# Kernel optimization log

Hardware: AMD Instinct MI355X
Metric: run time of the kernel (lower is better)

The kernel has to match this reference:

```python
import jax, jax.numpy as jnp
import numpy as np

N_HEADS = 16
MASK_NEG = -1e32


def setup_inputs() -> dict:
    key = jax.random.key(0)
    k0, k1, k2, k3, k4 = jax.random.split(key, 5)
    B, S, D = 8, 1024, 1024
    return {
        "q": jax.random.normal(k0, (B, S, D), dtype=jnp.float32),
        "k": jax.random.normal(k1, (B, S, D), dtype=jnp.float32),
        "v1": jax.random.normal(k2, (B, S, D), dtype=jnp.float32),
        "v2": jax.random.normal(k3, (B, S, D), dtype=jnp.float32),
        "counter_attention_mask": jax.random.randint(k4, (B, S), 0, 2, dtype=jnp.int32),
    }


def reference(q, k, v1, v2, counter_attention_mask):
    B, S, D = q.shape
    H = N_HEADS
    dk = D // H

    def split_heads(x):
        return x.reshape(B, S, H, dk).transpose(0, 2, 1, 3)  # [B,H,S,dk]

    qh, kh, v1h, v2h = split_heads(q), split_heads(k), split_heads(v1), split_heads(v2)

    # scaled dot-product scores [B,H,S,S]
    scores = jnp.einsum("bhqd,bhkd->bhqk", qh, kh) / jnp.sqrt(jnp.float32(dk))

    # create_mask(input, 0): allowed only where key_idx < query_idx (strict causal)
    i = jnp.arange(S)[:, None]
    j = jnp.arange(S)[None, :]
    allowed = j < i  # [S,S]
    scores = jnp.where(allowed[None, None], scores, MASK_NEG)

    # first softmax
    p = jax.nn.softmax(scores, axis=-1)

    # counter-attention mask: zero out masked key columns (per batch, all heads/rows)
    cm = counter_attention_mask[:, None, None, :]  # [B,1,1,S]
    p = jnp.where(cm == 1, jnp.float32(0.0), p)

    # second softmax over the (partially zeroed) probabilities
    p = jax.nn.softmax(p, axis=-1)

    # zero the first query row (pad_zero concat in the original)
    p = p.at[:, :, 0, :].set(0.0)

    out1 = jnp.einsum("bhqk,bhkd->bhqd", p, v1h)
    out2 = jnp.einsum("bhqk,bhkd->bhqd", p, v2h)

    def merge_heads(x):
        return x.transpose(0, 2, 1, 3).reshape(B, S, D)

    return merge_heads(out1), merge_heads(out2)
```

## Files before the change

### kernel.cpp

```cpp
#include <hip/hip_runtime.h>
#include <hip/hip_bf16.h>

#define B_ 8
#define S_ 1024
#define D_ 1024
#define H_ 16
#define DK_ 64
#define BH_ (B_ * H_)

typedef float f32x4 __attribute__((ext_vector_type(4)));
typedef short s16x8 __attribute__((ext_vector_type(8)));
typedef short s16x4 __attribute__((ext_vector_type(4)));

#define EXP2F(x) __builtin_amdgcn_exp2f(x)
#define LOG2F(x) __builtin_amdgcn_logf(x)
#define LOG2E 1.44269504088896f

static __device__ __forceinline__ short f2b(float f) {
  unsigned u = __builtin_bit_cast(unsigned, f);
  u = u + 0x7FFFu + ((u >> 16) & 1u);
  return (short)(u >> 16);
}
static __device__ __forceinline__ short f2bn(float f) {
  __hip_bfloat16 h = __float2bfloat16(f);
  return __builtin_bit_cast(short, h);
}

static __device__ __forceinline__ int slotf(int g, int e) {
  return (e < 4) ? (4 * g + e) : (16 + 4 * g + (e - 4));
}


__global__ __launch_bounds__(256) void prep_k(const float* __restrict__ k,
                                              short* __restrict__ kb) {
  const int bid = blockIdx.x;
  const int s0 = (bid & 63) * 16;
  const int b = bid >> 6;
  const int tid = threadIdx.x;
#pragma unroll
  for (int it = 0; it < 8; ++it) {
    int li = it * 256 + tid;
    int s = s0 + (li >> 7);
    int ch = li & 127;
    int h = ch >> 3;
    int dk0 = (ch & 7) * 8;
    const float* src = k + ((size_t)(b * S_ + s)) * D_ + ch * 8;
    s16x8 o;
#pragma unroll
    for (int e = 0; e < 8; ++e) o[e] = f2b(src[e]);
    *(s16x8*)(kb + ((size_t)((b * H_ + h) * S_ + s)) * DK_ + dk0) = o;
  }
}

__global__ __launch_bounds__(256) void prep_v(const float* __restrict__ v1,
                                              const float* __restrict__ v2,
                                              short* __restrict__ v1f,
                                              short* __restrict__ v2f,
                                              float* __restrict__ vs) {
  const int bid = blockIdx.x;
  const int sg = bid & 3;
  const int h = (bid >> 2) & 15;
  const int b = bid >> 6;
  const int tid = threadIdx.x;
  const int db = tid >> 6;
  const int lane = tid & 63;
  const int r = lane & 15;
  const int g = lane >> 4;
  const size_t inbase = (size_t)b * S_ * D_ + h * DK_ + db * 16 + r;
  float s1 = 0.f, s2 = 0.f;
#pragma unroll
  for (int it = 0; it < 8; ++it) {
    int jt = sg * 8 + it;
    int j0 = jt * 32;
    s16x8 o1, o2;
#pragma unroll
    for (int e = 0; e < 8; ++e) {
      int j = j0 + slotf(g, e);
      float a = v1[inbase + (size_t)j * D_];
      float c = v2[inbase + (size_t)j * D_];
      s1 += a;
      s2 += c;
      o1[e] = f2b(a);
      o2[e] = f2b(c);
    }
    size_t off = (((size_t)((b * H_ + h) * 32 + jt) * 4 + db) * 64 + lane) * 8;
    *(s16x8*)(v1f + off) = o1;
    *(s16x8*)(v2f + off) = o2;
  }
  s1 += __shfl_xor(s1, 16);
  s1 += __shfl_xor(s1, 32);
  s2 += __shfl_xor(s2, 16);
  s2 += __shfl_xor(s2, 32);
  if (g == 0) {
    int dd = db * 16 + r;
    atomicAdd(&vs[(size_t)b * D_ + h * DK_ + dd], s1);
    atomicAdd(&vs[(size_t)(B_ + b) * D_ + h * DK_ + dd], s2);
  }
}

__global__ __launch_bounds__(256, 2) void attn_fast6(
    const float* __restrict__ q, const short* __restrict__ kb,
    const short* __restrict__ v1f, const short* __restrict__ v2f,
    const int* __restrict__ cm, const float* __restrict__ vs,
    float* __restrict__ out) {
  const int bid = blockIdx.x;
  const int xcd = bid & 7;
  const int idx = bid >> 3;
  const int pr = idx & 7;
  const int bhgrp = idx >> 3;
  const int bh = bhgrp * 8 + xcd;
  const int b = bh >> 4, h = bh & 15;

  const int tid = threadIdx.x;
  const int wid = tid >> 6;
  const int lane = tid & 63;
  const int r = lane & 15;
  const int g = lane >> 4;

  const int aseg = 8 + pr;
  const int bseg = 7 - pr;
  const int qh = aseg * 64 + wid * 16;
  const int ql = bseg * 64 + (3 - wid) * 16;
  const int iqh = qh + r;
  const int iql = ql + r;
  const int njt = (aseg * 64 + 94) >> 5;

  __shared__ __align__(16) char sbuf[2][12288];
  __shared__ unsigned cmw[32];
  {
    const int* cmb = cm + b * S_;
#pragma unroll
    for (int it = 0; it < 4; ++it) {
      unsigned long long m = __ballot(cmb[it * 256 + tid] == 1);
      if (lane == 0) {
        int w0 = it * 8 + wid * 2;
        cmw[w0] = (unsigned)m;
        cmw[w0 + 1] = (unsigned)(m >> 32);
      }
    }
  }

  const float qscale = 0.125f * LOG2E;
  s16x8 qfh0, qfh1, qfl0, qfl1;
  {
    const float* qp = q + ((size_t)(b * S_ + qh + r)) * D_ + h * DK_;
#pragma unroll
    for (int e = 0; e < 8; ++e) qfh0[e] = f2bn(qp[8 * g + e] * qscale);
#pragma unroll
    for (int e = 0; e < 8; ++e) qfh1[e] = f2bn(qp[32 + 8 * g + e] * qscale);
    const float* qp2 = q + ((size_t)(b * S_ + ql + r)) * D_ + h * DK_;
#pragma unroll
    for (int e = 0; e < 8; ++e) qfl0[e] = f2bn(qp2[8 * g + e] * qscale);
#pragma unroll
    for (int e = 0; e < 8; ++e) qfl1[e] = f2bn(qp2[32 + 8 * g + e] * qscale);
  }

  const short* kbh = kb + (size_t)bh * S_ * DK_;
  const short* v1bh = v1f + (size_t)bh * 32 * 2048;
  const short* v2bh = v2f + (size_t)bh * 32 * 2048;

  const int srow = tid >> 3;
  const int sch = tid & 7;

#define SLK(reg, jtv) reg = *(const s16x8*)(kbh + (size_t)(jtv)*2048 + tid * 8);
#define SLV(d1, d2, jtv)                                           \
  {                                                                \
    d1 = *(const s16x8*)(v1bh + (size_t)(jtv)*2048 + tid * 8);     \
    d2 = *(const s16x8*)(v2bh + (size_t)(jtv)*2048 + tid * 8);     \
  }
#define SWK(buf, reg) \
  *(s16x8*)((buf) + srow * 128 + ((sch ^ (srow & 7)) * 16)) = reg;
#define SWV(buf, d1, d2)                        \
  {                                             \
    *(s16x8*)((buf) + 4096 + tid * 16) = d1;    \
    *(s16x8*)((buf) + 8192 + tid * 16) = d2;    \
  }
#define KFRAG(sK, row, quad) \
  (*(const s16x8*)((sK) + (row)*128 + (((quad) ^ ((row)&7)) * 16)))

  float Zh = 0.f, Zl = 0.f;
  {
    s16x8 rk;
    SLK(rk, 0);
    __syncthreads();
    SWK(sbuf[0], rk);
    __syncthreads();
    for (int jt = 0; jt < njt; ++jt) {
      const int jb = jt * 32;
      const char* sK = sbuf[jt & 1];
      const bool pf = (jt + 1 < njt);
      s16x8 rk2;
      if (pf) SLK(rk2, jt + 1);
      s16x8 k00 = KFRAG(sK, r, g);
      s16x8 k01 = KFRAG(sK, r, 4 + g);
      s16x8 k10 = KFRAG(sK, 16 + r, g);
      s16x8 k11 = KFRAG(sK, 16 + r, 4 + g);
      f32x4 s0 = {0.f, 0.f, 0.f, 0.f}, s1 = {0.f, 0.f, 0.f, 0.f};
      s0 = __builtin_amdgcn_mfma_f32_16x16x32_bf16(k00, qfh0, s0, 0, 0, 0);
      s0 = __builtin_amdgcn_mfma_f32_16x16x32_bf16(k01, qfh1, s0, 0, 0, 0);
      s1 = __builtin_amdgcn_mfma_f32_16x16x32_bf16(k10, qfh0, s1, 0, 0, 0);
      s1 = __builtin_amdgcn_mfma_f32_16x16x32_bf16(k11, qfh1, s1, 0, 0, 0);
#pragma unroll
      for (int e = 0; e < 4; ++e) {
        int j0 = jb + 4 * g + e, j1 = jb + 16 + 4 * g + e;
        Zh += (j0 < iqh) ? EXP2F(s0[e]) : 0.f;
        Zh += (j1 < iqh) ? EXP2F(s1[e]) : 0.f;
      }
      if (jb < ql + 16) {
        f32x4 t0 = {0.f, 0.f, 0.f, 0.f}, t1 = {0.f, 0.f, 0.f, 0.f};
        t0 = __builtin_amdgcn_mfma_f32_16x16x32_bf16(k00, qfl0, t0, 0, 0, 0);
        t0 = __builtin_amdgcn_mfma_f32_16x16x32_bf16(k01, qfl1, t0, 0, 0, 0);
        t1 = __builtin_amdgcn_mfma_f32_16x16x32_bf16(k10, qfl0, t1, 0, 0, 0);
        t1 = __builtin_amdgcn_mfma_f32_16x16x32_bf16(k11, qfl1, t1, 0, 0, 0);
#pragma unroll
        for (int e = 0; e < 4; ++e) {
          int j0 = jb + 4 * g + e, j1 = jb + 16 + 4 * g + e;
          Zl += (j0 < iql) ? EXP2F(t0[e]) : 0.f;
          Zl += (j1 < iql) ? EXP2F(t1[e]) : 0.f;
        }
      }
      if (pf) SWK(sbuf[(jt + 1) & 1], rk2);
      __syncthreads();
    }
  }
  Zh += __shfl_xor(Zh, 16);
  Zh += __shfl_xor(Zh, 32);
  Zl += __shfl_xor(Zl, 16);
  Zl += __shfl_xor(Zl, 32);
  const float lzh = -LOG2F(Zh);
  const float lzl = -LOG2F(Zl);

  f32x4 a1h[4], a2h[4], a1l[4], a2l[4];
#pragma unroll
  for (int d0 = 0; d0 < 4; ++d0) {
    a1h[d0] = (f32x4){0.f, 0.f, 0.f, 0.f};
    a2h[d0] = (f32x4){0.f, 0.f, 0.f, 0.f};
    a1l[d0] = (f32x4){0.f, 0.f, 0.f, 0.f};
    a2l[d0] = (f32x4){0.f, 0.f, 0.f, 0.f};
  }
  f32x4 wsh = {0.f, 0.f, 0.f, 0.f}, wsl = {0.f, 0.f, 0.f, 0.f};
  s16x8 ones;
#pragma unroll
  for (int e = 0; e < 8; ++e) ones[e] = (short)0x3F80;

  {
    s16x8 rk, rv1, rv2;
    SLK(rk, 0);
    SLV(rv1, rv2, 0);
    SWK(sbuf[0], rk);
    SWV(sbuf[0], rv1, rv2);
    __syncthreads();
    for (int jt = 0; jt < njt; ++jt) {
      const int jb = jt * 32;
      const char* sB = sbuf[jt & 1];
      const bool pf = (jt + 1 < njt);
      s16x8 rk2, rv12, rv22;
      if (pf) {
        SLK(rk2, jt + 1);
        SLV(rv12, rv22, jt + 1);
      }
      s16x8 k00 = KFRAG(sB, r, g);
      s16x8 k01 = KFRAG(sB, r, 4 + g);
      s16x8 k10 = KFRAG(sB, 16 + r, g);
      s16x8 k11 = KFRAG(sB, 16 + r, 4 + g);
      f32x4 s0 = {0.f, 0.f, 0.f, 0.f}, s1 = {0.f, 0.f, 0.f, 0.f};
      s0 = __builtin_amdgcn_mfma_f32_16x16x32_bf16(k00, qfh0, s0, 0, 0, 0);
      s0 = __builtin_amdgcn_mfma_f32_16x16x32_bf16(k01, qfh1, s0, 0, 0, 0);
      s1 = __builtin_amdgcn_mfma_f32_16x16x32_bf16(k10, qfh0, s1, 0, 0, 0);
      s1 = __builtin_amdgcn_mfma_f32_16x16x32_bf16(k11, qfh1, s1, 0, 0, 0);
      const bool bc = (jb < ql + 16);
      f32x4 t0, t1;
      if (bc) {
        t0 = (f32x4){0.f, 0.f, 0.f, 0.f};
        t1 = (f32x4){0.f, 0.f, 0.f, 0.f};
        t0 = __builtin_amdgcn_mfma_f32_16x16x32_bf16(k00, qfl0, t0, 0, 0, 0);
        t0 = __builtin_amdgcn_mfma_f32_16x16x32_bf16(k01, qfl1, t0, 0, 0, 0);
        t1 = __builtin_amdgcn_mfma_f32_16x16x32_bf16(k10, qfl0, t1, 0, 0, 0);
        t1 = __builtin_amdgcn_mfma_f32_16x16x32_bf16(k11, qfl1, t1, 0, 0, 0);
      }
      s16x8 vb1[4], vb2[4];
#pragma unroll
      for (int db = 0; db < 4; ++db) {
        vb1[db] = *(const s16x8*)(sB + 4096 + (db * 64 + lane) * 16);
        vb2[db] = *(const s16x8*)(sB + 8192 + (db * 64 + lane) * 16);
      }
      const unsigned cw = cmw[jt];
      int cmbit[8];
#pragma unroll
      for (int s2 = 0; s2 < 2; ++s2)
#pragma unroll
        for (int e = 0; e < 4; ++e)
          cmbit[s2 * 4 + e] = (int)((cw >> (s2 * 16 + 4 * g + e)) & 1u);
      s16x8 wah;
      {
        float wv[8];
#pragma unroll
        for (int s2 = 0; s2 < 2; ++s2) {
          f32x4 sv = s2 ? s1 : s0;
#pragma unroll
          for (int e = 0; e < 4; ++e) {
            int j = jb + s2 * 16 + 4 * g + e;
            float pe = EXP2F(sv[e] + lzh);
            float xe = EXP2F(pe * LOG2E) - 1.f;
            bool ok = !cmbit[s2 * 4 + e] && (j < iqh);
            wv[s2 * 4 + e] = ok ? xe : 0.f;
          }
        }
#pragma unroll
        for (int e = 0; e < 8; ++e) wah[e] = f2bn(wv[e]);
      }
      s16x8 wal;
      if (bc) {
        float wv[8];
#pragma unroll
        for (int s2 = 0; s2 < 2; ++s2) {
          f32x4 sv = s2 ? t1 : t0;
#pragma unroll
          for (int e = 0; e < 4; ++e) {
            int j = jb + s2 * 16 + 4 * g + e;
            float pe = EXP2F(sv[e] + lzl);
            float xe = EXP2F(pe * LOG2E) - 1.f;
            bool ok = !cmbit[s2 * 4 + e] && (j < iql);
            wv[s2 * 4 + e] = ok ? xe : 0.f;
          }
        }
#pragma unroll
        for (int e = 0; e < 8; ++e) wal[e] = f2bn(wv[e]);
      }
#pragma unroll
      for (int db = 0; db < 4; ++db) {
        a1h[db] = __builtin_amdgcn_mfma_f32_16x16x32_bf16(wah, vb1[db], a1h[db], 0, 0, 0);
        a2h[db] = __builtin_amdgcn_mfma_f32_16x16x32_bf16(wah, vb2[db], a2h[db], 0, 0, 0);
      }
      wsh = __builtin_amdgcn_mfma_f32_16x16x32_bf16(wah, ones, wsh, 0, 0, 0);
      if (bc) {
#pragma unroll
        for (int db = 0; db < 4; ++db) {
          a1l[db] = __builtin_amdgcn_mfma_f32_16x16x32_bf16(wal, vb1[db], a1l[db], 0, 0, 0);
          a2l[db] = __builtin_amdgcn_mfma_f32_16x16x32_bf16(wal, vb2[db], a2l[db], 0, 0, 0);
        }
        wsl = __builtin_amdgcn_mfma_f32_16x16x32_bf16(wal, ones, wsl, 0, 0, 0);
      }
      if (pf) {
        SWK(sbuf[(jt + 1) & 1], rk2);
        SWV(sbuf[(jt + 1) & 1], rv12, rv22);
      }
      __syncthreads();
    }
  }
#undef SLK
#undef SLV
#undef SWK
#undef SWV
#undef KFRAG

  float* out1 = out;
  float* out2 = out + (size_t)B_ * S_ * D_;
  const float* vs1 = vs + (size_t)b * D_ + h * DK_;
  const float* vs2 = vs + (size_t)(B_ + b) * D_ + h * DK_;

#pragma unroll
  for (int e = 0; e < 4; ++e) {
    {
      float inv = 1.f / ((float)S_ + wsh[e]);
      int io = qh + 4 * g + e;
      size_t ro = ((size_t)(b * S_) + io) * D_ + h * DK_;
#pragma unroll
      for (int db = 0; db < 4; ++db) {
        int dd = db * 16 + r;
        out1[ro + dd] = (a1h[db][e] + vs1[dd]) * inv;
        out2[ro + dd] = (a2h[db][e] + vs2[dd]) * inv;
      }
    }
    {
      float inv = 1.f / ((float)S_ + wsl[e]);
      int io = ql + 4 * g + e;
      bool zero = (io == 0);
      size_t ro = ((size_t)(b * S_) + io) * D_ + h * DK_;
#pragma unroll
      for (int db = 0; db < 4; ++db) {
        int dd = db * 16 + r;
        out1[ro + dd] = zero ? 0.f : (a1l[db][e] + vs1[dd]) * inv;
        out2[ro + dd] = zero ? 0.f : (a2l[db][e] + vs2[dd]) * inv;
      }
    }
  }
}


__global__ __launch_bounds__(256) void vsum_kernel(const float* __restrict__ v1,
                                                   const float* __restrict__ v2,
                                                   float* __restrict__ vs) {
  int bid = blockIdx.x;
  int sc = bid & 7, dc = (bid >> 3) & 3, b = bid >> 5;
  int d = dc * 256 + threadIdx.x;
  const float* p1 = v1 + ((size_t)b * S_ + sc * 128) * D_ + d;
  const float* p2 = v2 + ((size_t)b * S_ + sc * 128) * D_ + d;
  float s1 = 0.f, s2 = 0.f;
  for (int j = 0; j < 128; ++j) {
    s1 += p1[(size_t)j * D_];
    s2 += p2[(size_t)j * D_];
  }
  atomicAdd(&vs[b * D_ + d], s1);
  atomicAdd(&vs[B_ * D_ + b * D_ + d], s2);
}

__global__ __launch_bounds__(256) void dualattn_fallback(
    const float* __restrict__ q, const float* __restrict__ k,
    const float* __restrict__ v1, const float* __restrict__ v2,
    const int* __restrict__ cm, const float* __restrict__ vs,
    float* __restrict__ out) {
  const int bid = blockIdx.x;
  const int qt = bid & 15;
  const int h = (bid >> 4) & 15;
  const int b = bid >> 8;
  const int tid = threadIdx.x;
  const int wid = tid >> 6;
  const int lane = tid & 63;
  const int r = lane & 15;
  const int g = lane >> 4;
  const int qw = qt * 64 + wid * 16;
  const int iq = qw + r;

  __shared__ __align__(16) char kbuf[32 * 128];
  __shared__ __align__(16) char vtb1[64 * 64];
  __shared__ __align__(16) char vtb2[64 * 64];
  __shared__ unsigned cmw[32];

  {
    const int* cmb = cm + b * S_;
#pragma unroll
    for (int it = 0; it < 4; ++it) {
      int c = cmb[it * 256 + tid];
      unsigned long long m = __ballot(c == 1);
      if (lane == 0) {
        int w0 = (it * 256 + wid * 64) >> 5;
        cmw[w0] = (unsigned)m;
        cmw[w0 + 1] = (unsigned)(m >> 32);
      }
    }
  }

  s16x8 qf0, qf1;
  {
    const float* qp = q + ((size_t)(b * S_) + qw + r) * D_ + h * DK_;
#pragma unroll
    for (int e = 0; e < 8; ++e) qf0[e] = f2b(qp[8 * g + e] * 0.125f);
#pragma unroll
    for (int e = 0; e < 8; ++e) qf1[e] = f2b(qp[32 + 8 * g + e] * 0.125f);
  }

  const int njt = 2 * qt + 2;
  const float* kbase = k + (size_t)(b * S_) * D_ + h * DK_;
  const float* v1base = v1 + (size_t)(b * S_) * D_ + h * DK_;
  const float* v2base = v2 + (size_t)(b * S_) * D_ + h * DK_;
  const int srow = tid >> 3;
  const int sch = tid & 7;

  float m1 = -INFINITY, Z1 = 0.f;
  for (int jt = 0; jt < njt; ++jt) {
    const int jbase = jt * 32;
    __syncthreads();
    {
      const float* kr = kbase + (size_t)(jbase + srow) * D_ + sch * 8;
      s16x8 pk;
#pragma unroll
      for (int e = 0; e < 8; ++e) pk[e] = f2b(kr[e]);
      *(s16x8*)(kbuf + srow * 128 + ((sch ^ (srow & 7)) * 16)) = pk;
    }
    __syncthreads();
    if (jbase < qw + 16) {
#pragma unroll
      for (int sub = 0; sub < 2; ++sub) {
        const int jsb = jbase + sub * 16;
        if (jsb < qw + 16) {
          const int row = sub * 16 + r;
          s16x8 ka0 = *(const s16x8*)(kbuf + row * 128 + ((g ^ (row & 7)) * 16));
          s16x8 ka1 = *(const s16x8*)(kbuf + row * 128 + (((4 + g) ^ (row & 7)) * 16));
          f32x4 sv = {0.f, 0.f, 0.f, 0.f};
          sv = __builtin_amdgcn_mfma_f32_16x16x32_bf16(ka0, qf0, sv, 0, 0, 0);
          sv = __builtin_amdgcn_mfma_f32_16x16x32_bf16(ka1, qf1, sv, 0, 0, 0);
          float tm = m1;
#pragma unroll
          for (int e = 0; e < 4; ++e) {
            int j = jsb + 4 * g + e;
            if (j < iq) tm = fmaxf(tm, sv[e]);
          }
          if (tm > m1) { Z1 *= __expf(m1 - tm); m1 = tm; }
#pragma unroll
          for (int e = 0; e < 4; ++e) {
            int j = jsb + 4 * g + e;
            if (j < iq) Z1 += __expf(sv[e] - tm);
          }
        }
      }
    }
  }
#pragma unroll
  for (int off = 16; off < 64; off <<= 1) {
    float mo = __shfl_xor(m1, off);
    float zo = __shfl_xor(Z1, off);
    float mn = fmaxf(m1, mo);
    if (mn > -INFINITY) {
      Z1 = Z1 * __expf(m1 - mn) + zo * __expf(mo - mn);
      m1 = mn;
    }
  }
  float z1i;
  if (m1 > -INFINITY) { z1i = 1.f / Z1; }
  else { z1i = 0.f; m1 = 0.f; }

  f32x4 acc1[4], acc2[4];
#pragma unroll
  for (int d0 = 0; d0 < 4; ++d0) {
    acc1[d0] = (f32x4){0.f, 0.f, 0.f, 0.f};
    acc2[d0] = (f32x4){0.f, 0.f, 0.f, 0.f};
  }
  float wsum = 0.f;

  for (int jt = 0; jt < njt; ++jt) {
    const int jbase = jt * 32;
    __syncthreads();
    {
      const float* kr = kbase + (size_t)(jbase + srow) * D_ + sch * 8;
      s16x8 pk;
#pragma unroll
      for (int e = 0; e < 8; ++e) pk[e] = f2b(kr[e]);
      *(s16x8*)(kbuf + srow * 128 + ((sch ^ (srow & 7)) * 16)) = pk;
      const float* v1r = v1base + (size_t)(jbase + srow) * D_ + sch * 8;
      const float* v2r = v2base + (size_t)(jbase + srow) * D_ + sch * 8;
#pragma unroll
      for (int e = 0; e < 8; ++e) {
        int dd = sch * 8 + e;
        int off = dd * 64 + (((srow >> 2) ^ (dd & 7)) * 8) + (srow & 3) * 2;
        *(short*)(vtb1 + off) = f2b(v1r[e]);
        *(short*)(vtb2 + off) = f2b(v2r[e]);
      }
    }
    __syncthreads();
    if (jbase < qw + 16) {
      const unsigned cmword = cmw[jbase >> 5];
      float w[8];
#pragma unroll
      for (int sub = 0; sub < 2; ++sub) {
        const int jsb = jbase + sub * 16;
        if (jsb < qw + 16) {
          const int row = sub * 16 + r;
          s16x8 ka0 = *(const s16x8*)(kbuf + row * 128 + ((g ^ (row & 7)) * 16));
          s16x8 ka1 = *(const s16x8*)(kbuf + row * 128 + (((4 + g) ^ (row & 7)) * 16));
          f32x4 sv = {0.f, 0.f, 0.f, 0.f};
          sv = __builtin_amdgcn_mfma_f32_16x16x32_bf16(ka0, qf0, sv, 0, 0, 0);
          sv = __builtin_amdgcn_mfma_f32_16x16x32_bf16(ka1, qf1, sv, 0, 0, 0);
#pragma unroll
          for (int e = 0; e < 4; ++e) {
            int j = jsb + 4 * g + e;
            float x = 0.f;
            if (j < iq && !((cmword >> (j & 31)) & 1u)) {
              float p = __expf(sv[e] - m1) * z1i;
              x = __expf(p) - 1.f;
            }
            w[sub * 4 + e] = x;
            wsum += x;
          }
        } else {
#pragma unroll
          for (int e = 0; e < 4; ++e) w[sub * 4 + e] = 0.f;
        }
      }
      s16x8 wa;
#pragma unroll
      for (int e = 0; e < 8; ++e) wa[e] = f2b(w[e]);
#pragma unroll
      for (int db = 0; db < 4; ++db) {
        const int dd = db * 16 + r;
        const int off0 = dd * 64 + ((g ^ (dd & 7)) * 8);
        const int off1 = dd * 64 + (((4 + g) ^ (dd & 7)) * 8);
        s16x4 lo1 = *(const s16x4*)(vtb1 + off0);
        s16x4 hi1 = *(const s16x4*)(vtb1 + off1);
        s16x8 vb1 = __builtin_shufflevector(lo1, hi1, 0, 1, 2, 3, 4, 5, 6, 7);
        acc1[db] = __builtin_amdgcn_mfma_f32_16x16x32_bf16(wa, vb1, acc1[db], 0, 0, 0);
        s16x4 lo2 = *(const s16x4*)(vtb2 + off0);
        s16x4 hi2 = *(const s16x4*)(vtb2 + off1);
        s16x8 vb2 = __builtin_shufflevector(lo2, hi2, 0, 1, 2, 3, 4, 5, 6, 7);
        acc2[db] = __builtin_amdgcn_mfma_f32_16x16x32_bf16(wa, vb2, acc2[db], 0, 0, 0);
      }
    }
  }

  wsum += __shfl_xor(wsum, 16);
  wsum += __shfl_xor(wsum, 32);
  const float z2 = (float)S_ + wsum;

  float* out1 = out;
  float* out2 = out + (size_t)B_ * S_ * D_;
#pragma unroll
  for (int e = 0; e < 4; ++e) {
    float z2e = __shfl(z2, 4 * g + e);
    float inv = 1.f / z2e;
    int io = qw + 4 * g + e;
    bool zero = (io == 0);
    size_t ro = ((size_t)(b * S_) + io) * D_ + h * DK_;
#pragma unroll
    for (int db = 0; db < 4; ++db) {
      int dd = db * 16 + r;
      float c1 = vs[(size_t)b * D_ + h * DK_ + dd];
      float c2 = vs[(size_t)(B_ + b) * D_ + h * DK_ + dd];
      out1[ro + dd] = zero ? 0.f : (acc1[db][e] + c1) * inv;
      out2[ro + dd] = zero ? 0.f : (acc2[db][e] + c2) * inv;
    }
  }
}


extern "C" void kernel_launch(void* const* d_in, const int* in_sizes, int n_in,
                              void* d_out, int out_size, void* d_ws, size_t ws_size,
                              hipStream_t stream) {
  (void)in_sizes; (void)n_in; (void)out_size;
  const float* q = (const float*)d_in[0];
  const float* k = (const float*)d_in[1];
  const float* v1 = (const float*)d_in[2];
  const float* v2 = (const float*)d_in[3];
  const int* cm = (const int*)d_in[4];
  float* outp = (float*)d_out;

  const size_t VS_BYTES = 2 * B_ * D_ * sizeof(float);
  const size_t FRAG_SHORTS = (size_t)BH_ * S_ * DK_;
  const size_t FRAG_BYTES = FRAG_SHORTS * 2;
  const size_t NEED = VS_BYTES + 3 * FRAG_BYTES;

  float* vs = (float*)d_ws;
  (void)hipMemsetAsync(vs, 0, VS_BYTES, stream);

  if (ws_size >= NEED) {
    short* kb = (short*)((char*)d_ws + VS_BYTES);
    short* v1f = kb + FRAG_SHORTS;
    short* v2f = v1f + FRAG_SHORTS;
    prep_k<<<B_ * (S_ / 16), 256, 0, stream>>>(k, kb);
    prep_v<<<B_ * H_ * 4, 256, 0, stream>>>(v1, v2, v1f, v2f, vs);
    attn_fast6<<<1024, 256, 0, stream>>>(q, kb, v1f, v2f, cm, vs, outp);
  } else {
    vsum_kernel<<<256, 256, 0, stream>>>(v1, v2, vs);
    dualattn_fallback<<<B_ * H_ * 16, 256, 0, stream>>>(q, k, v1, v2, cm, vs, outp);
  }
}
```

Baseline: 117.8 us.

## Double key tile to 64 rows per sync and skip causal checks off-diagonal

The attention kernel now stages 64 keys per shared-memory tile instead of 32, doubling the double buffers to 24 KB each and running two 32-key subtiles per iteration. This halves the number of barriers and loop iterations in both the normalizer pass and the accumulation pass. The causal index comparison is now applied only on the diagonal tile (jt == aseg or jt == bseg), which removes per-element compares elsewhere. The cost is more LDS per block (about 48 KB), which could limit occupancy, and more prefetch registers per thread.

Result: faster. 108.9 us (-7.6%).

```diff
diff --git a/kernel.cpp b/kernel.cpp
--- a/kernel.cpp
+++ b/kernel.cpp
@@ -98,7 +98,7 @@
   }
 }
 
-__global__ __launch_bounds__(256, 2) void attn_fast6(
+__global__ __launch_bounds__(256, 2) void attn_fast7(
     const float* __restrict__ q, const short* __restrict__ kb,
     const short* __restrict__ v1f, const short* __restrict__ v2f,
     const int* __restrict__ cm, const float* __restrict__ vs,
@@ -123,9 +123,9 @@
   const int ql = bseg * 64 + (3 - wid) * 16;
   const int iqh = qh + r;
   const int iql = ql + r;
-  const int njt = (aseg * 64 + 94) >> 5;
-
-  __shared__ __align__(16) char sbuf[2][12288];
+  const int njt = aseg + 1;
+
+  __shared__ __align__(16) char sbuf[2][24576];
   __shared__ unsigned cmw[32];
   {
     const int* cmb = cm + b * S_;
@@ -159,67 +159,97 @@
   const short* v1bh = v1f + (size_t)bh * 32 * 2048;
   const short* v2bh = v2f + (size_t)bh * 32 * 2048;
 
-  const int srow = tid >> 3;
-  const int sch = tid & 7;
-
-#define SLK(reg, jtv) reg = *(const s16x8*)(kbh + (size_t)(jtv)*2048 + tid * 8);
-#define SLV(d1, d2, jtv)                                           \
-  {                                                                \
-    d1 = *(const s16x8*)(v1bh + (size_t)(jtv)*2048 + tid * 8);     \
-    d2 = *(const s16x8*)(v2bh + (size_t)(jtv)*2048 + tid * 8);     \
-  }
-#define SWK(buf, reg) \
-  *(s16x8*)((buf) + srow * 128 + ((sch ^ (srow & 7)) * 16)) = reg;
-#define SWV(buf, d1, d2)                        \
-  {                                             \
-    *(s16x8*)((buf) + 4096 + tid * 16) = d1;    \
-    *(s16x8*)((buf) + 8192 + tid * 16) = d2;    \
+  const int r0s = tid >> 3, c0s = tid & 7;
+  const int r1s = (tid + 256) >> 3, c1s = tid & 7;
+
+#define SLK(g0, g1, jtv)                                          \
+  {                                                               \
+    const short* kp = kbh + (size_t)(jtv) * 4096;                 \
+    g0 = *(const s16x8*)(kp + tid * 8);                           \
+    g1 = *(const s16x8*)(kp + (tid + 256) * 8);                   \
+  }
+#define SWK(buf, g0, g1)                                          \
+  {                                                               \
+    *(s16x8*)((buf) + r0s * 128 + ((c0s ^ (r0s & 7)) * 16)) = g0; \
+    *(s16x8*)((buf) + r1s * 128 + ((c1s ^ (r1s & 7)) * 16)) = g1; \
+  }
+#define SLV(a0, a1, b0, b1, jtv)                                  \
+  {                                                               \
+    const short* p1 = v1bh + (size_t)(jtv) * 4096;                \
+    const short* p2 = v2bh + (size_t)(jtv) * 4096;                \
+    a0 = *(const s16x8*)(p1 + tid * 8);                           \
+    a1 = *(const s16x8*)(p1 + (tid + 256) * 8);                   \
+    b0 = *(const s16x8*)(p2 + tid * 8);                           \
+    b1 = *(const s16x8*)(p2 + (tid + 256) * 8);                   \
+  }
+#define SWV(buf, a0, a1, b0, b1)                                  \
+  {                                                               \
+    *(s16x8*)((buf) + 8192 + tid * 16) = a0;                      \
+    *(s16x8*)((buf) + 8192 + (tid + 256) * 16) = a1;              \
+    *(s16x8*)((buf) + 16384 + tid * 16) = b0;                     \
+    *(s16x8*)((buf) + 16384 + (tid + 256) * 16) = b1;             \
   }
 #define KFRAG(sK, row, quad) \
   (*(const s16x8*)((sK) + (row)*128 + (((quad) ^ ((row)&7)) * 16)))
 
   float Zh = 0.f, Zl = 0.f;
   {
-    s16x8 rk;
-    SLK(rk, 0);
+    s16x8 rk0, rk1;
+    SLK(rk0, rk1, 0);
     __syncthreads();
-    SWK(sbuf[0], rk);
+    SWK(sbuf[0], rk0, rk1);
     __syncthreads();
     for (int jt = 0; jt < njt; ++jt) {
-      const int jb = jt * 32;
       const char* sK = sbuf[jt & 1];
       const bool pf = (jt + 1 < njt);
-      s16x8 rk2;
-      if (pf) SLK(rk2, jt + 1);
-      s16x8 k00 = KFRAG(sK, r, g);
-      s16x8 k01 = KFRAG(sK, r, 4 + g);
-      s16x8 k10 = KFRAG(sK, 16 + r, g);
-      s16x8 k11 = KFRAG(sK, 16 + r, 4 + g);
-      f32x4 s0 = {0.f, 0.f, 0.f, 0.f}, s1 = {0.f, 0.f, 0.f, 0.f};
-      s0 = __builtin_amdgcn_mfma_f32_16x16x32_bf16(k00, qfh0, s0, 0, 0, 0);
-      s0 = __builtin_amdgcn_mfma_f32_16x16x32_bf16(k01, qfh1, s0, 0, 0, 0);
-      s1 = __builtin_amdgcn_mfma_f32_16x16x32_bf16(k10, qfh0, s1, 0, 0, 0);
-      s1 = __builtin_amdgcn_mfma_f32_16x16x32_bf16(k11, qfh1, s1, 0, 0, 0);
-#pragma unroll
-      for (int e = 0; e < 4; ++e) {
-        int j0 = jb + 4 * g + e, j1 = jb + 16 + 4 * g + e;
-        Zh += (j0 < iqh) ? EXP2F(s0[e]) : 0.f;
-        Zh += (j1 < iqh) ? EXP2F(s1[e]) : 0.f;
-      }
-      if (jb < ql + 16) {
-        f32x4 t0 = {0.f, 0.f, 0.f, 0.f}, t1 = {0.f, 0.f, 0.f, 0.f};
-        t0 = __builtin_amdgcn_mfma_f32_16x16x32_bf16(k00, qfl0, t0, 0, 0, 0);
-        t0 = __builtin_amdgcn_mfma_f32_16x16x32_bf16(k01, qfl1, t0, 0, 0, 0);
-        t1 = __builtin_amdgcn_mfma_f32_16x16x32_bf16(k10, qfl0, t1, 0, 0, 0);
-        t1 = __builtin_amdgcn_mfma_f32_16x16x32_bf16(k11, qfl1, t1, 0, 0, 0);
-#pragma unroll
-        for (int e = 0; e < 4; ++e) {
-          int j0 = jb + 4 * g + e, j1 = jb + 16 + 4 * g + e;
-          Zl += (j0 < iql) ? EXP2F(t0[e]) : 0.f;
-          Zl += (j1 < iql) ? EXP2F(t1[e]) : 0.f;
-        }
-      }
-      if (pf) SWK(sbuf[(jt + 1) & 1], rk2);
+      s16x8 nk0, nk1;
+      if (pf) SLK(nk0, nk1, jt + 1);
+      const bool chB = (jt == aseg);
+      const bool clB = (jt == bseg);
+#pragma unroll
+      for (int sub = 0; sub < 2; ++sub) {
+        const int jsb = jt * 64 + sub * 32;
+        const int row0 = sub * 32 + r, row1 = row0 + 16;
+        s16x8 k00 = KFRAG(sK, row0, g);
+        s16x8 k01 = KFRAG(sK, row0, 4 + g);
+        s16x8 k10 = KFRAG(sK, row1, g);
+        s16x8 k11 = KFRAG(sK, row1, 4 + g);
+        f32x4 s0 = {0.f, 0.f, 0.f, 0.f}, s1 = {0.f, 0.f, 0.f, 0.f};
+        s0 = __builtin_amdgcn_mfma_f32_16x16x32_bf16(k00, qfh0, s0, 0, 0, 0);
+        s0 = __builtin_amdgcn_mfma_f32_16x16x32_bf16(k01, qfh1, s0, 0, 0, 0);
+        s1 = __builtin_amdgcn_mfma_f32_16x16x32_bf16(k10, qfh0, s1, 0, 0, 0);
+        s1 = __builtin_amdgcn_mfma_f32_16x16x32_bf16(k11, qfh1, s1, 0, 0, 0);
+        if (chB) {
+#pragma unroll
+          for (int e = 0; e < 4; ++e) {
+            int j0 = jsb + 4 * g + e, j1 = jsb + 16 + 4 * g + e;
+            Zh += (j0 < iqh) ? EXP2F(s0[e]) : 0.f;
+            Zh += (j1 < iqh) ? EXP2F(s1[e]) : 0.f;
+          }
+        } else {
+#pragma unroll
+          for (int e = 0; e < 4; ++e) Zh += EXP2F(s0[e]) + EXP2F(s1[e]);
+        }
+        if (jsb < ql + 16) {
+          f32x4 t0 = {0.f, 0.f, 0.f, 0.f}, t1 = {0.f, 0.f, 0.f, 0.f};
+          t0 = __builtin_amdgcn_mfma_f32_16x16x32_bf16(k00, qfl0, t0, 0, 0, 0);
+          t0 = __builtin_amdgcn_mfma_f32_16x16x32_bf16(k01, qfl1, t0, 0, 0, 0);
+          t1 = __builtin_amdgcn_mfma_f32_16x16x32_bf16(k10, qfl0, t1, 0, 0, 0);
+          t1 = __builtin_amdgcn_mfma_f32_16x16x32_bf16(k11, qfl1, t1, 0, 0, 0);
+          if (clB) {
+#pragma unroll
+            for (int e = 0; e < 4; ++e) {
+              int j0 = jsb + 4 * g + e, j1 = jsb + 16 + 4 * g + e;
+              Zl += (j0 < iql) ? EXP2F(t0[e]) : 0.f;
+              Zl += (j1 < iql) ? EXP2F(t1[e]) : 0.f;
+            }
+          } else {
+#pragma unroll
+            for (int e = 0; e < 4; ++e) Zl += EXP2F(t0[e]) + EXP2F(t1[e]);
+          }
+        }
+      }
+      if (pf) SWK(sbuf[(jt + 1) & 1], nk0, nk1);
       __syncthreads();
     }
   }
@@ -244,106 +274,116 @@
   for (int e = 0; e < 8; ++e) ones[e] = (short)0x3F80;
 
   {
-    s16x8 rk, rv1, rv2;
-    SLK(rk, 0);
-    SLV(rv1, rv2, 0);
-    SWK(sbuf[0], rk);
-    SWV(sbuf[0], rv1, rv2);
+    s16x8 rk0, rk1, ra0, ra1, rb0, rb1;
+    SLK(rk0, rk1, 0);
+    SLV(ra0, ra1, rb0, rb1, 0);
+    SWK(sbuf[0], rk0, rk1);
+    SWV(sbuf[0], ra0, ra1, rb0, rb1);
     __syncthreads();
     for (int jt = 0; jt < njt; ++jt) {
-      const int jb = jt * 32;
       const char* sB = sbuf[jt & 1];
       const bool pf = (jt + 1 < njt);
-      s16x8 rk2, rv12, rv22;
+      s16x8 nk0, nk1, na0, na1, nb0, nb1;
       if (pf) {
-        SLK(rk2, jt + 1);
-        SLV(rv12, rv22, jt + 1);
-      }
-      s16x8 k00 = KFRAG(sB, r, g);
-      s16x8 k01 = KFRAG(sB, r, 4 + g);
-      s16x8 k10 = KFRAG(sB, 16 + r, g);
-      s16x8 k11 = KFRAG(sB, 16 + r, 4 + g);
-      f32x4 s0 = {0.f, 0.f, 0.f, 0.f}, s1 = {0.f, 0.f, 0.f, 0.f};
-      s0 = __builtin_amdgcn_mfma_f32_16x16x32_bf16(k00, qfh0, s0, 0, 0, 0);
-      s0 = __builtin_amdgcn_mfma_f32_16x16x32_bf16(k01, qfh1, s0, 0, 0, 0);
-      s1 = __builtin_amdgcn_mfma_f32_16x16x32_bf16(k10, qfh0, s1, 0, 0, 0);
-      s1 = __builtin_amdgcn_mfma_f32_16x16x32_bf16(k11, qfh1, s1, 0, 0, 0);
-      const bool bc = (jb < ql + 16);
-      f32x4 t0, t1;
-      if (bc) {
-        t0 = (f32x4){0.f, 0.f, 0.f, 0.f};
-        t1 = (f32x4){0.f, 0.f, 0.f, 0.f};
-        t0 = __builtin_amdgcn_mfma_f32_16x16x32_bf16(k00, qfl0, t0, 0, 0, 0);
-        t0 = __builtin_amdgcn_mfma_f32_16x16x32_bf16(k01, qfl1, t0, 0, 0, 0);
-        t1 = __builtin_amdgcn_mfma_f32_16x16x32_bf16(k10, qfl0, t1, 0, 0, 0);
-        t1 = __builtin_amdgcn_mfma_f32_16x16x32_bf16(k11, qfl1, t1, 0, 0, 0);
-      }
-      s16x8 vb1[4], vb2[4];
-#pragma unroll
-      for (int db = 0; db < 4; ++db) {
-        vb1[db] = *(const s16x8*)(sB + 4096 + (db * 64 + lane) * 16);
-        vb2[db] = *(const s16x8*)(sB + 8192 + (db * 64 + lane) * 16);
-      }
-      const unsigned cw = cmw[jt];
-      int cmbit[8];
-#pragma unroll
-      for (int s2 = 0; s2 < 2; ++s2)
-#pragma unroll
-        for (int e = 0; e < 4; ++e)
-          cmbit[s2 * 4 + e] = (int)((cw >> (s2 * 16 + 4 * g + e)) & 1u);
-      s16x8 wah;
-      {
-        float wv[8];
-#pragma unroll
-        for (int s2 = 0; s2 < 2; ++s2) {
-          f32x4 sv = s2 ? s1 : s0;
-#pragma unroll
-          for (int e = 0; e < 4; ++e) {
-            int j = jb + s2 * 16 + 4 * g + e;
-            float pe = EXP2F(sv[e] + lzh);
-            float xe = EXP2F(pe * LOG2E) - 1.f;
-            bool ok = !cmbit[s2 * 4 + e] && (j < iqh);
-            wv[s2 * 4 + e] = ok ? xe : 0.f;
-          }
-        }
-#pragma unroll
-        for (int e = 0; e < 8; ++e) wah[e] = f2bn(wv[e]);
-      }
-      s16x8 wal;
-      if (bc) {
-        float wv[8];
-#pragma unroll
-        for (int s2 = 0; s2 < 2; ++s2) {
-          f32x4 sv = s2 ? t1 : t0;
-#pragma unroll
-          for (int e = 0; e < 4; ++e) {
-            int j = jb + s2 * 16 + 4 * g + e;
-            float pe = EXP2F(sv[e] + lzl);
-            float xe = EXP2F(pe * LOG2E) - 1.f;
-            bool ok = !cmbit[s2 * 4 + e] && (j < iql);
-            wv[s2 * 4 + e] = ok ? xe : 0.f;
-          }
-        }
-#pragma unroll
-        for (int e = 0; e < 8; ++e) wal[e] = f2bn(wv[e]);
-      }
-#pragma unroll
-      for (int db = 0; db < 4; ++db) {
-        a1h[db] = __builtin_amdgcn_mfma_f32_16x16x32_bf16(wah, vb1[db], a1h[db], 0, 0, 0);
-        a2h[db] = __builtin_amdgcn_mfma_f32_16x16x32_bf16(wah, vb2[db], a2h[db], 0, 0, 0);
-      }
-      wsh = __builtin_amdgcn_mfma_f32_16x16x32_bf16(wah, ones, wsh, 0, 0, 0);
-      if (bc) {
+        SLK(nk0, nk1, jt + 1);
+        SLV(na0, na1, nb0, nb1, jt + 1);
+      }
+      const bool chB = (jt == aseg);
+      const bool clB = (jt == bseg);
+#pragma unroll
+      for (int sub = 0; sub < 2; ++sub) {
+        const int jsb = jt * 64 + sub * 32;
+        const int row0 = sub * 32 + r, row1 = row0 + 16;
+        s16x8 k00 = KFRAG(sB, row0, g);
+        s16x8 k01 = KFRAG(sB, row0, 4 + g);
+        s16x8 k10 = KFRAG(sB, row1, g);
+        s16x8 k11 = KFRAG(sB, row1, 4 + g);
+        f32x4 s0 = {0.f, 0.f, 0.f, 0.f}, s1 = {0.f, 0.f, 0.f, 0.f};
+        s0 = __builtin_amdgcn_mfma_f32_16x16x32_bf16(k00, qfh0, s0, 0, 0, 0);
+        s0 = __builtin_amdgcn_mfma_f32_16x16x32_bf16(k01, qfh1, s0, 0, 0, 0);
+        s1 = __builtin_amdgcn_mfma_f32_16x16x32_bf16(k10, qfh0, s1, 0, 0, 0);
+        s1 = __builtin_amdgcn_mfma_f32_16x16x32_bf16(k11, qfh1, s1, 0, 0, 0);
+        const bool bc = (jsb < ql + 16);
+        f32x4 t0, t1;
+        if (bc) {
+          t0 = (f32x4){0.f, 0.f, 0.f, 0.f};
+          t1 = (f32x4){0.f, 0.f, 0.f, 0.f};
+          t0 = __builtin_amdgcn_mfma_f32_16x16x32_bf16(k00, qfl0, t0, 0, 0, 0);
+          t0 = __builtin_amdgcn_mfma_f32_16x16x32_bf16(k01, qfl1, t0, 0, 0, 0);
+          t1 = __builtin_amdgcn_mfma_f32_16x16x32_bf16(k10, qfl0, t1, 0, 0, 0);
+          t1 = __builtin_amdgcn_mfma_f32_16x16x32_bf16(k11, qfl1, t1, 0, 0, 0);
+        }
+        const unsigned cw = cmw[2 * jt + sub];
+        int cmbit[8];
+#pragma unroll
+        for (int s2 = 0; s2 < 2; ++s2)
+#pragma unroll
+          for (int e = 0; e < 4; ++e)
+            cmbit[s2 * 4 + e] = (int)((cw >> (s2 * 16 + 4 * g + e)) & 1u);
+        s16x8 wah;
+        {
+          float wv[8];
+#pragma unroll
+          for (int s2 = 0; s2 < 2; ++s2) {
+            f32x4 sv = s2 ? s1 : s0;
+#pragma unroll
+            for (int e = 0; e < 4; ++e) {
+              int j = jsb + s2 * 16 + 4 * g + e;
+              float pe = EXP2F(sv[e] + lzh);
+              float xe = EXP2F(pe * LOG2E) - 1.f;
+              bool ok = !cmbit[s2 * 4 + e];
+              if (chB) ok = ok && (j < iqh);
+              wv[s2 * 4 + e] = ok ? xe : 0.f;
+            }
+          }
+#pragma unroll
+          for (int e = 0; e < 8; ++e) wah[e] = f2bn(wv[e]);
+        }
+        s16x8 wal;
+        if (bc) {
+          float wv[8];
+#pragma unroll
+          for (int s2 = 0; s2 < 2; ++s2) {
+            f32x4 sv = s2 ? t1 : t0;
+#pragma unroll
+            for (int e = 0; e < 4; ++e) {
+              int j = jsb + s2 * 16 + 4 * g + e;
+              float pe = EXP2F(sv[e] + lzl);
+              float xe = EXP2F(pe * LOG2E) - 1.f;
+              bool ok = !cmbit[s2 * 4 + e];
+              if (clB) ok = ok && (j < iql);
+              wv[s2 * 4 + e] = ok ? xe : 0.f;
+            }
+          }
+#pragma unroll
+          for (int e = 0; e < 8; ++e) wal[e] = f2bn(wv[e]);
+        }
+        const char* vb1p = sB + 8192 + sub * 4096;
+        const char* vb2p = sB + 16384 + sub * 4096;
+        s16x8 vb1[4], vb2[4];
 #pragma unroll
         for (int db = 0; db < 4; ++db) {
-          a1l[db] = __builtin_amdgcn_mfma_f32_16x16x32_bf16(wal, vb1[db], a1l[db], 0, 0, 0);
-          a2l[db] = __builtin_amdgcn_mfma_f32_16x16x32_bf16(wal, vb2[db], a2l[db], 0, 0, 0);
-        }
-        wsl = __builtin_amdgcn_mfma_f32_16x16x32_bf16(wal, ones, wsl, 0, 0, 0);
+          vb1[db] = *(const s16x8*)(vb1p + (db * 64 + lane) * 16);
+          vb2[db] = *(const s16x8*)(vb2p + (db * 64 + lane) * 16);
+        }
+#pragma unroll
+        for (int db = 0; db < 4; ++db) {
+          a1h[db] = __builtin_amdgcn_mfma_f32_16x16x32_bf16(wah, vb1[db], a1h[db], 0, 0, 0);
+          a2h[db] = __builtin_amdgcn_mfma_f32_16x16x32_bf16(wah, vb2[db], a2h[db], 0, 0, 0);
+        }
+        wsh = __builtin_amdgcn_mfma_f32_16x16x32_bf16(wah, ones, wsh, 0, 0, 0);
+        if (bc) {
+#pragma unroll
+          for (int db = 0; db < 4; ++db) {
+            a1l[db] = __builtin_amdgcn_mfma_f32_16x16x32_bf16(wal, vb1[db], a1l[db], 0, 0, 0);
+            a2l[db] = __builtin_amdgcn_mfma_f32_16x16x32_bf16(wal, vb2[db], a2l[db], 0, 0, 0);
+          }
+          wsl = __builtin_amdgcn_mfma_f32_16x16x32_bf16(wal, ones, wsl, 0, 0, 0);
+        }
       }
       if (pf) {
-        SWK(sbuf[(jt + 1) & 1], rk2);
-        SWV(sbuf[(jt + 1) & 1], rv12, rv22);
+        SWK(sbuf[(jt + 1) & 1], nk0, nk1);
+        SWV(sbuf[(jt + 1) & 1], na0, na1, nb0, nb1);
       }
       __syncthreads();
     }
@@ -637,7 +677,7 @@
     short* v2f = v1f + FRAG_SHORTS;
     prep_k<<<B_ * (S_ / 16), 256, 0, stream>>>(k, kb);
     prep_v<<<B_ * H_ * 4, 256, 0, stream>>>(v1, v2, v1f, v2f, vs);
-    attn_fast6<<<1024, 256, 0, stream>>>(q, kb, v1f, v2f, cm, vs, outp);
+    attn_fast7<<<1024, 256, 0, stream>>>(q, kb, v1f, v2f, cm, vs, outp);
   } else {
     vsum_kernel<<<256, 256, 0, stream>>>(v1, v2, vs);
     dualattn_fallback<<<B_ * H_ * 16, 256, 0, stream>>>(q, k, v1, v2, cm, vs, outp);
```

## Replace paired causal query tiles with one tile per block, heaviest first

Applied to the files above, without the earlier changes.

The attention kernel no longer pairs a high and a low 64-row query segment per block for causal load balancing. Each block now handles a single segment, the grid doubles to 2048 blocks, and blocks are ordered from the longest segment down. Register use per thread roughly halves, so launch bounds go from 2 to 4 waves per SIMD to raise occupancy. Per-wave tiles above the diagonal are skipped and masking is applied only near it. The trade is more blocks and more repeated K/V streaming from global memory for better occupancy and scheduling.

Measured after the change: 135.4 us. 1.15x slower.

```diff
diff --git a/kernel.cpp b/kernel.cpp
--- a/kernel.cpp
+++ b/kernel.cpp
@@ -98,7 +98,7 @@
   }
 }
 
-__global__ __launch_bounds__(256, 2) void attn_fast6(
+__global__ __launch_bounds__(256, 4) void attn_fastA(
     const float* __restrict__ q, const short* __restrict__ kb,
     const short* __restrict__ v1f, const short* __restrict__ v2f,
     const int* __restrict__ cm, const float* __restrict__ vs,
@@ -106,8 +106,8 @@
   const int bid = blockIdx.x;
   const int xcd = bid & 7;
   const int idx = bid >> 3;
-  const int pr = idx & 7;
-  const int bhgrp = idx >> 3;
+  const int seg = 15 - (idx & 15);
+  const int bhgrp = idx >> 4;
   const int bh = bhgrp * 8 + xcd;
   const int b = bh >> 4, h = bh & 15;
 
@@ -117,13 +117,9 @@
   const int r = lane & 15;
   const int g = lane >> 4;
 
-  const int aseg = 8 + pr;
-  const int bseg = 7 - pr;
-  const int qh = aseg * 64 + wid * 16;
-  const int ql = bseg * 64 + (3 - wid) * 16;
-  const int iqh = qh + r;
-  const int iql = ql + r;
-  const int njt = (aseg * 64 + 94) >> 5;
+  const int qw = seg * 64 + wid * 16;
+  const int iq = qw + r;
+  const int njt = 2 * seg + 2;
 
   __shared__ __align__(16) char sbuf[2][12288];
   __shared__ unsigned cmw[32];
@@ -141,18 +137,13 @@
   }
 
   const float qscale = 0.125f * LOG2E;
-  s16x8 qfh0, qfh1, qfl0, qfl1;
+  s16x8 qf0, qf1;
   {
-    const float* qp = q + ((size_t)(b * S_ + qh + r)) * D_ + h * DK_;
-#pragma unroll
-    for (int e = 0; e < 8; ++e) qfh0[e] = f2bn(qp[8 * g + e] * qscale);
-#pragma unroll
-    for (int e = 0; e < 8; ++e) qfh1[e] = f2bn(qp[32 + 8 * g + e] * qscale);
-    const float* qp2 = q + ((size_t)(b * S_ + ql + r)) * D_ + h * DK_;
-#pragma unroll
-    for (int e = 0; e < 8; ++e) qfl0[e] = f2bn(qp2[8 * g + e] * qscale);
-#pragma unroll
-    for (int e = 0; e < 8; ++e) qfl1[e] = f2bn(qp2[32 + 8 * g + e] * qscale);
+    const float* qp = q + ((size_t)(b * S_ + qw + r)) * D_ + h * DK_;
+#pragma unroll
+    for (int e = 0; e < 8; ++e) qf0[e] = f2bn(qp[8 * g + e] * qscale);
+#pragma unroll
+    for (int e = 0; e < 8; ++e) qf1[e] = f2bn(qp[32 + 8 * g + e] * qscale);
   }
 
   const short* kbh = kb + (size_t)bh * S_ * DK_;
@@ -178,7 +169,7 @@
 #define KFRAG(sK, row, quad) \
   (*(const s16x8*)((sK) + (row)*128 + (((quad) ^ ((row)&7)) * 16)))
 
-  float Zh = 0.f, Zl = 0.f;
+  float Z = 0.f;
   {
     s16x8 rk;
     SLK(rk, 0);
@@ -191,54 +182,43 @@
       const bool pf = (jt + 1 < njt);
       s16x8 rk2;
       if (pf) SLK(rk2, jt + 1);
-      s16x8 k00 = KFRAG(sK, r, g);
-      s16x8 k01 = KFRAG(sK, r, 4 + g);
-      s16x8 k10 = KFRAG(sK, 16 + r, g);
-      s16x8 k11 = KFRAG(sK, 16 + r, 4 + g);
-      f32x4 s0 = {0.f, 0.f, 0.f, 0.f}, s1 = {0.f, 0.f, 0.f, 0.f};
-      s0 = __builtin_amdgcn_mfma_f32_16x16x32_bf16(k00, qfh0, s0, 0, 0, 0);
-      s0 = __builtin_amdgcn_mfma_f32_16x16x32_bf16(k01, qfh1, s0, 0, 0, 0);
-      s1 = __builtin_amdgcn_mfma_f32_16x16x32_bf16(k10, qfh0, s1, 0, 0, 0);
-      s1 = __builtin_amdgcn_mfma_f32_16x16x32_bf16(k11, qfh1, s1, 0, 0, 0);
-#pragma unroll
-      for (int e = 0; e < 4; ++e) {
-        int j0 = jb + 4 * g + e, j1 = jb + 16 + 4 * g + e;
-        Zh += (j0 < iqh) ? EXP2F(s0[e]) : 0.f;
-        Zh += (j1 < iqh) ? EXP2F(s1[e]) : 0.f;
-      }
-      if (jb < ql + 16) {
-        f32x4 t0 = {0.f, 0.f, 0.f, 0.f}, t1 = {0.f, 0.f, 0.f, 0.f};
-        t0 = __builtin_amdgcn_mfma_f32_16x16x32_bf16(k00, qfl0, t0, 0, 0, 0);
-        t0 = __builtin_amdgcn_mfma_f32_16x16x32_bf16(k01, qfl1, t0, 0, 0, 0);
-        t1 = __builtin_amdgcn_mfma_f32_16x16x32_bf16(k10, qfl0, t1, 0, 0, 0);
-        t1 = __builtin_amdgcn_mfma_f32_16x16x32_bf16(k11, qfl1, t1, 0, 0, 0);
-#pragma unroll
-        for (int e = 0; e < 4; ++e) {
-          int j0 = jb + 4 * g + e, j1 = jb + 16 + 4 * g + e;
-          Zl += (j0 < iql) ? EXP2F(t0[e]) : 0.f;
-          Zl += (j1 < iql) ? EXP2F(t1[e]) : 0.f;
+      if (jb < qw + 16) {
+        s16x8 k00 = KFRAG(sK, r, g);
+        s16x8 k01 = KFRAG(sK, r, 4 + g);
+        s16x8 k10 = KFRAG(sK, 16 + r, g);
+        s16x8 k11 = KFRAG(sK, 16 + r, 4 + g);
+        f32x4 s0 = {0.f, 0.f, 0.f, 0.f}, s1 = {0.f, 0.f, 0.f, 0.f};
+        s0 = __builtin_amdgcn_mfma_f32_16x16x32_bf16(k00, qf0, s0, 0, 0, 0);
+        s0 = __builtin_amdgcn_mfma_f32_16x16x32_bf16(k01, qf1, s0, 0, 0, 0);
+        s1 = __builtin_amdgcn_mfma_f32_16x16x32_bf16(k10, qf0, s1, 0, 0, 0);
+        s1 = __builtin_amdgcn_mfma_f32_16x16x32_bf16(k11, qf1, s1, 0, 0, 0);
+        if (jb + 31 >= qw) {
+#pragma unroll
+          for (int e = 0; e < 4; ++e) {
+            int j0 = jb + 4 * g + e, j1 = jb + 16 + 4 * g + e;
+            Z += (j0 < iq) ? EXP2F(s0[e]) : 0.f;
+            Z += (j1 < iq) ? EXP2F(s1[e]) : 0.f;
+          }
+        } else {
+#pragma unroll
+          for (int e = 0; e < 4; ++e) Z += EXP2F(s0[e]) + EXP2F(s1[e]);
         }
       }
       if (pf) SWK(sbuf[(jt + 1) & 1], rk2);
       __syncthreads();
     }
   }
-  Zh += __shfl_xor(Zh, 16);
-  Zh += __shfl_xor(Zh, 32);
-  Zl += __shfl_xor(Zl, 16);
-  Zl += __shfl_xor(Zl, 32);
-  const float lzh = -LOG2F(Zh);
-  const float lzl = -LOG2F(Zl);
-
-  f32x4 a1h[4], a2h[4], a1l[4], a2l[4];
+  Z += __shfl_xor(Z, 16);
+  Z += __shfl_xor(Z, 32);
+  const float lz = -LOG2F(Z);
+
+  f32x4 a1[4], a2[4];
 #pragma unroll
   for (int d0 = 0; d0 < 4; ++d0) {
-    a1h[d0] = (f32x4){0.f, 0.f, 0.f, 0.f};
-    a2h[d0] = (f32x4){0.f, 0.f, 0.f, 0.f};
-    a1l[d0] = (f32x4){0.f, 0.f, 0.f, 0.f};
-    a2l[d0] = (f32x4){0.f, 0.f, 0.f, 0.f};
-  }
-  f32x4 wsh = {0.f, 0.f, 0.f, 0.f}, wsl = {0.f, 0.f, 0.f, 0.f};
+    a1[d0] = (f32x4){0.f, 0.f, 0.f, 0.f};
+    a2[d0] = (f32x4){0.f, 0.f, 0.f, 0.f};
+  }
+  f32x4 ws = {0.f, 0.f, 0.f, 0.f};
   s16x8 ones;
 #pragma unroll
   for (int e = 0; e < 8; ++e) ones[e] = (short)0x3F80;
@@ -259,87 +239,49 @@
         SLK(rk2, jt + 1);
         SLV(rv12, rv22, jt + 1);
       }
-      s16x8 k00 = KFRAG(sB, r, g);
-      s16x8 k01 = KFRAG(sB, r, 4 + g);
-      s16x8 k10 = KFRAG(sB, 16 + r, g);
-      s16x8 k11 = KFRAG(sB, 16 + r, 4 + g);
-      f32x4 s0 = {0.f, 0.f, 0.f, 0.f}, s1 = {0.f, 0.f, 0.f, 0.f};
-      s0 = __builtin_amdgcn_mfma_f32_16x16x32_bf16(k00, qfh0, s0, 0, 0, 0);
-      s0 = __builtin_amdgcn_mfma_f32_16x16x32_bf16(k01, qfh1, s0, 0, 0, 0);
-      s1 = __builtin_amdgcn_mfma_f32_16x16x32_bf16(k10, qfh0, s1, 0, 0, 0);
-      s1 = __builtin_amdgcn_mfma_f32_16x16x32_bf16(k11, qfh1, s1, 0, 0, 0);
-      const bool bc = (jb < ql + 16);
-      f32x4 t0, t1;
-      if (bc) {
-        t0 = (f32x4){0.f, 0.f, 0.f, 0.f};
-        t1 = (f32x4){0.f, 0.f, 0.f, 0.f};
-        t0 = __builtin_amdgcn_mfma_f32_16x16x32_bf16(k00, qfl0, t0, 0, 0, 0);
-        t0 = __builtin_amdgcn_mfma_f32_16x16x32_bf16(k01, qfl1, t0, 0, 0, 0);
-        t1 = __builtin_amdgcn_mfma_f32_16x16x32_bf16(k10, qfl0, t1, 0, 0, 0);
-        t1 = __builtin_amdgcn_mfma_f32_16x16x32_bf16(k11, qfl1, t1, 0, 0, 0);
-      }
-      s16x8 vb1[4], vb2[4];
-#pragma unroll
-      for (int db = 0; db < 4; ++db) {
-        vb1[db] = *(const s16x8*)(sB + 4096 + (db * 64 + lane) * 16);
-        vb2[db] = *(const s16x8*)(sB + 8192 + (db * 64 + lane) * 16);
-      }
-      const unsigned cw = cmw[jt];
-      int cmbit[8];
-#pragma unroll
-      for (int s2 = 0; s2 < 2; ++s2)
-#pragma unroll
-        for (int e = 0; e < 4; ++e)
-          cmbit[s2 * 4 + e] = (int)((cw >> (s2 * 16 + 4 * g + e)) & 1u);
-      s16x8 wah;
-      {
-        float wv[8];
-#pragma unroll
-        for (int s2 = 0; s2 < 2; ++s2) {
-          f32x4 sv = s2 ? s1 : s0;
-#pragma unroll
-          for (int e = 0; e < 4; ++e) {
-            int j = jb + s2 * 16 + 4 * g + e;
-            float pe = EXP2F(sv[e] + lzh);
-            float xe = EXP2F(pe * LOG2E) - 1.f;
-            bool ok = !cmbit[s2 * 4 + e] && (j < iqh);
-            wv[s2 * 4 + e] = ok ? xe : 0.f;
+      if (jb < qw + 16) {
+        s16x8 k00 = KFRAG(sB, r, g);
+        s16x8 k01 = KFRAG(sB, r, 4 + g);
+        s16x8 k10 = KFRAG(sB, 16 + r, g);
+        s16x8 k11 = KFRAG(sB, 16 + r, 4 + g);
+        f32x4 s0 = {0.f, 0.f, 0.f, 0.f}, s1 = {0.f, 0.f, 0.f, 0.f};
+        s0 = __builtin_amdgcn_mfma_f32_16x16x32_bf16(k00, qf0, s0, 0, 0, 0);
+        s0 = __builtin_amdgcn_mfma_f32_16x16x32_bf16(k01, qf1, s0, 0, 0, 0);
+        s1 = __builtin_amdgcn_mfma_f32_16x16x32_bf16(k10, qf0, s1, 0, 0, 0);
+        s1 = __builtin_amdgcn_mfma_f32_16x16x32_bf16(k11, qf1, s1, 0, 0, 0);
+        const unsigned cw = cmw[jt];
+        const bool cb = (jb + 31 >= qw);
+        s16x8 wa;
+        {
+          float wv[8];
+#pragma unroll
+          for (int s2 = 0; s2 < 2; ++s2) {
+            f32x4 sv = s2 ? s1 : s0;
+#pragma unroll
+            for (int e = 0; e < 4; ++e) {
+              int j = jb + s2 * 16 + 4 * g + e;
+              float pe = EXP2F(sv[e] + lz);
+              float xe = EXP2F(pe * LOG2E) - 1.f;
+              bool ok = !((cw >> (s2 * 16 + 4 * g + e)) & 1u);
+              if (cb) ok = ok && (j < iq);
+              wv[s2 * 4 + e] = ok ? xe : 0.f;
+            }
           }
+#pragma unroll
+          for (int e = 0; e < 8; ++e) wa[e] = f2bn(wv[e]);
         }
-#pragma unroll
-        for (int e = 0; e < 8; ++e) wah[e] = f2bn(wv[e]);
-      }
-      s16x8 wal;
-      if (bc) {
-        float wv[8];
-#pragma unroll
-        for (int s2 = 0; s2 < 2; ++s2) {
-          f32x4 sv = s2 ? t1 : t0;
-#pragma unroll
-          for (int e = 0; e < 4; ++e) {
-            int j = jb + s2 * 16 + 4 * g + e;
-            float pe = EXP2F(sv[e] + lzl);
-            float xe = EXP2F(pe * LOG2E) - 1.f;
-            bool ok = !cmbit[s2 * 4 + e] && (j < iql);
-            wv[s2 * 4 + e] = ok ? xe : 0.f;
-          }
+        s16x8 vb1[4], vb2[4];
+#pragma unroll
+        for (int db = 0; db < 4; ++db) {
+          vb1[db] = *(const s16x8*)(sB + 4096 + (db * 64 + lane) * 16);
+          vb2[db] = *(const s16x8*)(sB + 8192 + (db * 64 + lane) * 16);
         }
 #pragma unroll
-        for (int e = 0; e < 8; ++e) wal[e] = f2bn(wv[e]);
-      }
-#pragma unroll
-      for (int db = 0; db < 4; ++db) {
-        a1h[db] = __builtin_amdgcn_mfma_f32_16x16x32_bf16(wah, vb1[db], a1h[db], 0, 0, 0);
-        a2h[db] = __builtin_amdgcn_mfma_f32_16x16x32_bf16(wah, vb2[db], a2h[db], 0, 0, 0);
-      }
-      wsh = __builtin_amdgcn_mfma_f32_16x16x32_bf16(wah, ones, wsh, 0, 0, 0);
-      if (bc) {
-#pragma unroll
         for (int db = 0; db < 4; ++db) {
-          a1l[db] = __builtin_amdgcn_mfma_f32_16x16x32_bf16(wal, vb1[db], a1l[db], 0, 0, 0);
-          a2l[db] = __builtin_amdgcn_mfma_f32_16x16x32_bf16(wal, vb2[db], a2l[db], 0, 0, 0);
+          a1[db] = __builtin_amdgcn_mfma_f32_16x16x32_bf16(wa, vb1[db], a1[db], 0, 0, 0);
+          a2[db] = __builtin_amdgcn_mfma_f32_16x16x32_bf16(wa, vb2[db], a2[db], 0, 0, 0);
         }
-        wsl = __builtin_amdgcn_mfma_f32_16x16x32_bf16(wal, ones, wsl, 0, 0, 0);
+        ws = __builtin_amdgcn_mfma_f32_16x16x32_bf16(wa, ones, ws, 0, 0, 0);
       }
       if (pf) {
         SWK(sbuf[(jt + 1) & 1], rk2);
@@ -361,28 +303,15 @@
 
 #pragma unroll
   for (int e = 0; e < 4; ++e) {
-    {
-      float inv = 1.f / ((float)S_ + wsh[e]);
-      int io = qh + 4 * g + e;
-      size_t ro = ((size_t)(b * S_) + io) * D_ + h * DK_;
-#pragma unroll
-      for (int db = 0; db < 4; ++db) {
-        int dd = db * 16 + r;
-        out1[ro + dd] = (a1h[db][e] + vs1[dd]) * inv;
-        out2[ro + dd] = (a2h[db][e] + vs2[dd]) * inv;
-      }
-    }
-    {
-      float inv = 1.f / ((float)S_ + wsl[e]);
-      int io = ql + 4 * g + e;
-      bool zero = (io == 0);
-      size_t ro = ((size_t)(b * S_) + io) * D_ + h * DK_;
-#pragma unroll
-      for (int db = 0; db < 4; ++db) {
-        int dd = db * 16 + r;
-        out1[ro + dd] = zero ? 0.f : (a1l[db][e] + vs1[dd]) * inv;
-        out2[ro + dd] = zero ? 0.f : (a2l[db][e] + vs2[dd]) * inv;
-      }
+    float inv = 1.f / ((float)S_ + ws[e]);
+    int io = qw + 4 * g + e;
+    bool zero = (io == 0);
+    size_t ro = ((size_t)(b * S_) + io) * D_ + h * DK_;
+#pragma unroll
+    for (int db = 0; db < 4; ++db) {
+      int dd = db * 16 + r;
+      out1[ro + dd] = zero ? 0.f : (a1[db][e] + vs1[dd]) * inv;
+      out2[ro + dd] = zero ? 0.f : (a2[db][e] + vs2[dd]) * inv;
     }
   }
 }
@@ -637,7 +566,7 @@
     short* v2f = v1f + FRAG_SHORTS;
     prep_k<<<B_ * (S_ / 16), 256, 0, stream>>>(k, kb);
     prep_v<<<B_ * H_ * 4, 256, 0, stream>>>(v1, v2, v1f, v2f, vs);
-    attn_fast6<<<1024, 256, 0, stream>>>(q, kb, v1f, v2f, cm, vs, outp);
+    attn_fastA<<<2048, 256, 0, stream>>>(q, kb, v1f, v2f, cm, vs, outp);
   } else {
     vsum_kernel<<<256, 256, 0, stream>>>(v1, v2, vs);
     dualattn_fallback<<<B_ * H_ * 16, 256, 0, stream>>>(q, k, v1, v2, cm, vs, outp);
```
